# Kernel optimization log

Measured on AMD Instinct MI355X. Metric: run time of the kernel, lower is better.

## Reference

```python
import jax, jax.numpy as jnp
import numpy as np

LAMBDA = 1.0

def _patches3x3(x):
    # x: [B, C, H, W] -> [B, C, 3, 3, H, W] of 3x3 zero-padded neighborhoods
    B, C, H, W = x.shape
    xp = jnp.pad(x, ((0, 0), (0, 0), (1, 1), (1, 1)))
    rows = []
    for i in range(3):
        cols = [xp[:, :, i:i + H, j:j + W] for j in range(3)]
        rows.append(jnp.stack(cols, axis=2))  # [B, C, 3, H, W]
    return jnp.stack(rows, axis=2)  # [B, C, 3, 3, H, W]


def setup_inputs() -> dict:
    key = jax.random.key(0)
    kU, kV, kW = jax.random.split(key, 3)
    B, Cin, Cout, H, W = 8, 16, 16, 224, 224
    U = jax.random.normal(kU, (B, Cin, H, W), dtype=jnp.float32)
    V = jax.random.normal(kV, (B, Cin, H, W), dtype=jnp.float32)
    # nn.init.uniform_(weight, -0.1, 0.1)
    weight = jax.random.uniform(kW, (Cout, Cin, 3, 3), dtype=jnp.float32,
                                minval=-0.1, maxval=0.1)
    return {"U": U, "V": V, "weight": weight}


def reference(U, V, weight):
    # u1_u2 / v1_v2: 3x3 neighborhood minus center pixel, per input channel
    u_diff = _patches3x3(U) - U[:, :, None, None, :, :]  # [B,C,3,3,H,W]
    v_diff = _patches3x3(V) - V[:, :, None, None, :, :]
    inv_l2 = 1.0 / (LAMBDA * LAMBDA)
    # S = 1 / sqrt(1 + |v1-v2|^2 / lambda^2)
    S = jax.lax.rsqrt(1.0 + v_diff * v_diff * inv_l2)
    # out[b,o,h,w] = sum_{c,ki,kj} weight[o,c,ki,kj] * S * u_diff
    out = jnp.einsum('ocij,bcijhw->bohw', weight, S * u_diff)
    return out
```

## Files before the change

kernel.cpp:

```cpp
#include <hip/hip_runtime.h>


constexpr int Bn = 8, Ci = 16, Co = 16, H = 224, W = 224;
constexpr int HW = H * W;

typedef _Float16 f16x8 __attribute__((ext_vector_type(8)));
typedef float    f32x4 __attribute__((ext_vector_type(4)));

template <bool EDGE>
__device__ __forceinline__ void load_row(const float* __restrict__ plane,
                                         int h, int w, float r[3]) {
  if (!EDGE) {
    const float* q = plane + h * W + w;
    r[0] = q[-1]; r[1] = q[0]; r[2] = q[1];
  } else {
    if ((unsigned)h < (unsigned)H) {
      const float* q = plane + h * W + w;
      r[0] = (w >= 1)     ? q[-1] : 0.0f;
      r[1] = q[0];
      r[2] = (w + 1 < W) ? q[1] : 0.0f;
    } else {
      r[0] = 0.0f; r[1] = 0.0f; r[2] = 0.0f;
    }
  }
}

template <bool EDGE>
__device__ __forceinline__ void sdconv_wave(
    const float* __restrict__ U, const float* __restrict__ V,
    const float* __restrict__ Wg, float* __restrict__ Out,
    int b, int h0, int w0, int lane) {
  const int px = lane & 15;
  const int cg = lane >> 4;

  const int w = w0 + px;

  f16x8 bfrag[4];
#pragma unroll
  for (int kc = 0; kc < 4; ++kc) {
    const int c = 4 * kc + cg;
    const float* wp = Wg + (px * Ci + c) * 9;
#pragma unroll
    for (int j = 0; j < 8; ++j) {
      const int tap = (j < 4) ? j : j + 1;
      bfrag[kc][j] = (_Float16)wp[tap];
    }
  }

  f32x4 d[4];
#pragma unroll
  for (int r = 0; r < 4; ++r) { d[r][0] = 0.f; d[r][1] = 0.f; d[r][2] = 0.f; d[r][3] = 0.f; }

#pragma unroll
  for (int kc = 0; kc < 4; ++kc) {
    const int c = 4 * kc + cg;
    const float* up = U + ((size_t)(b * Ci + c)) * HW;
    const float* vp = V + ((size_t)(b * Ci + c)) * HW;

    float u[3][3], v[3][3];
    load_row<EDGE>(up, h0 - 1, w, u[0]);
    load_row<EDGE>(vp, h0 - 1, w, v[0]);
    load_row<EDGE>(up, h0,     w, u[1]);
    load_row<EDGE>(vp, h0,     w, v[1]);

#pragma unroll
    for (int r = 0; r < 4; ++r) {
      load_row<EDGE>(up, h0 + r + 1, w, u[2]);
      load_row<EDGE>(vp, h0 + r + 1, w, v[2]);

      const float uc = u[1][1], vc = v[1][1];
      f16x8 a;
      int j = 0;
#pragma unroll
      for (int dh = 0; dh < 3; ++dh) {
#pragma unroll
        for (int dw = 0; dw < 3; ++dw) {
          if (dh == 1 && dw == 1) continue;
          const float vd = v[dh][dw] - vc;
          const float s  = rsqrtf(fmaf(vd, vd, 1.0f));
          a[j++] = (_Float16)(s * (u[dh][dw] - uc));
        }
      }
      d[r] = __builtin_amdgcn_mfma_f32_16x16x32_f16(a, bfrag[kc], d[r], 0, 0, 0);

#pragma unroll
      for (int i = 0; i < 3; ++i) {
        u[0][i] = u[1][i]; u[1][i] = u[2][i];
        v[0][i] = v[1][i]; v[1][i] = v[2][i];
      }
    }
  }

  const int wst = w0 + 4 * cg;
  const int o   = px;
#pragma unroll
  for (int r = 0; r < 4; ++r) {
    float* op = Out + (((size_t)b * Co + o) * H + (h0 + r)) * W + wst;
    *reinterpret_cast<f32x4*>(op) = d[r];
  }
}

__global__ __launch_bounds__(128)
void sdconv_mfma(const float* __restrict__ U, const float* __restrict__ V,
                 const float* __restrict__ Wg, float* __restrict__ Out) {
  const int lane = threadIdx.x & 63;
  const int wv   = threadIdx.x >> 6;
  const int w0 = blockIdx.x * 16;
  const int h0 = blockIdx.y * 8 + wv * 4;
  const int b  = blockIdx.z;

  const bool edge = (blockIdx.x == 0) | (blockIdx.x == gridDim.x - 1) |
                    (blockIdx.y == 0) | (blockIdx.y == gridDim.y - 1);
  if (edge)
    sdconv_wave<true >(U, V, Wg, Out, b, h0, w0, lane);
  else
    sdconv_wave<false>(U, V, Wg, Out, b, h0, w0, lane);
}

extern "C" void kernel_launch(void* const* d_in, const int* in_sizes, int n_in,
                              void* d_out, int out_size, void* d_ws, size_t ws_size,
                              hipStream_t stream) {
  const float* U  = (const float*)d_in[0];
  const float* V  = (const float*)d_in[1];
  const float* Wg = (const float*)d_in[2];
  float* Out = (float*)d_out;

  dim3 grid(W / 16, H / 8, Bn);
  dim3 block(128);
  sdconv_mfma<<<grid, block, 0, stream>>>(U, V, Wg, Out);
}
```

Baseline: 125.7 us.

## Process eight rows per wave with channel-interleaved rolling window and raw rsq

Each wave now computes eight output rows instead of four, which halves the grid and reduces the redundant halo-row reloads per output row. The loop order is swapped so that each output row loads the new input row for all four channel groups first and then issues the four MFMAs. The rolling three-row window is indexed with modular slots instead of shifting registers. rsqrtf is replaced by the raw hardware rsq builtin to drop any extra precision handling. The trade-off is higher register pressure from holding eight accumulators and four channel windows, and fewer blocks available for occupancy.

After: 119.8 us. -4.7%, faster.

```diff
diff --git a/kernel.cpp b/kernel.cpp
--- a/kernel.cpp
+++ b/kernel.cpp
@@ -3,13 +3,14 @@
 
 constexpr int Bn = 8, Ci = 16, Co = 16, H = 224, W = 224;
 constexpr int HW = H * W;
+constexpr int ROWS = 8;
 
 typedef _Float16 f16x8 __attribute__((ext_vector_type(8)));
 typedef float    f32x4 __attribute__((ext_vector_type(4)));
 
 template <bool EDGE>
 __device__ __forceinline__ void load_row(const float* __restrict__ plane,
-                                         int h, int w, float r[3]) {
+                                         int h, int w, float* __restrict__ r) {
   if (!EDGE) {
     const float* q = plane + h * W + w;
     r[0] = q[-1]; r[1] = q[0]; r[2] = q[1];
@@ -32,8 +33,7 @@
     int b, int h0, int w0, int lane) {
   const int px = lane & 15;
   const int cg = lane >> 4;
-
-  const int w = w0 + px;
+  const int w  = w0 + px;
 
   f16x8 bfrag[4];
 #pragma unroll
@@ -47,28 +47,44 @@
     }
   }
 
-  f32x4 d[4];
+  f32x4 d[ROWS];
 #pragma unroll
-  for (int r = 0; r < 4; ++r) { d[r][0] = 0.f; d[r][1] = 0.f; d[r][2] = 0.f; d[r][3] = 0.f; }
+  for (int r = 0; r < ROWS; ++r) d[r] = (f32x4){0.f, 0.f, 0.f, 0.f};
 
+  const float* up[4];
+  const float* vp[4];
 #pragma unroll
   for (int kc = 0; kc < 4; ++kc) {
     const int c = 4 * kc + cg;
-    const float* up = U + ((size_t)(b * Ci + c)) * HW;
-    const float* vp = V + ((size_t)(b * Ci + c)) * HW;
+    up[kc] = U + ((size_t)(b * Ci + c)) * HW;
+    vp[kc] = V + ((size_t)(b * Ci + c)) * HW;
+  }
 
-    float u[3][3], v[3][3];
-    load_row<EDGE>(up, h0 - 1, w, u[0]);
-    load_row<EDGE>(vp, h0 - 1, w, v[0]);
-    load_row<EDGE>(up, h0,     w, u[1]);
-    load_row<EDGE>(vp, h0,     w, v[1]);
+  float u[4][3][3], v[4][3][3];
+#pragma unroll
+  for (int kc = 0; kc < 4; ++kc) {
+    load_row<EDGE>(up[kc], h0 - 1, w, u[kc][0]);
+    load_row<EDGE>(vp[kc], h0 - 1, w, v[kc][0]);
+    load_row<EDGE>(up[kc], h0,     w, u[kc][1]);
+    load_row<EDGE>(vp[kc], h0,     w, v[kc][1]);
+  }
 
 #pragma unroll
-    for (int r = 0; r < 4; ++r) {
-      load_row<EDGE>(up, h0 + r + 1, w, u[2]);
-      load_row<EDGE>(vp, h0 + r + 1, w, v[2]);
+  for (int r = 0; r < ROWS; ++r) {
+    const int st = r % 3;
+    const int sm = (r + 1) % 3;
+    const int sb = (r + 2) % 3;
 
-      const float uc = u[1][1], vc = v[1][1];
+#pragma unroll
+    for (int kc = 0; kc < 4; ++kc) {
+      load_row<EDGE>(up[kc], h0 + r + 1, w, u[kc][sb]);
+      load_row<EDGE>(vp[kc], h0 + r + 1, w, v[kc][sb]);
+    }
+
+#pragma unroll
+    for (int kc = 0; kc < 4; ++kc) {
+      const float uc = u[kc][sm][1], vc = v[kc][sm][1];
+      const int slot[3] = {st, sm, sb};
       f16x8 a;
       int j = 0;
 #pragma unroll
@@ -76,25 +92,19 @@
 #pragma unroll
         for (int dw = 0; dw < 3; ++dw) {
           if (dh == 1 && dw == 1) continue;
-          const float vd = v[dh][dw] - vc;
-          const float s  = rsqrtf(fmaf(vd, vd, 1.0f));
-          a[j++] = (_Float16)(s * (u[dh][dw] - uc));
+          const float vd = v[kc][slot[dh]][dw] - vc;
+          const float s  = __builtin_amdgcn_rsqf(fmaf(vd, vd, 1.0f));
+          a[j++] = (_Float16)(s * (u[kc][slot[dh]][dw] - uc));
         }
       }
       d[r] = __builtin_amdgcn_mfma_f32_16x16x32_f16(a, bfrag[kc], d[r], 0, 0, 0);
-
-#pragma unroll
-      for (int i = 0; i < 3; ++i) {
-        u[0][i] = u[1][i]; u[1][i] = u[2][i];
-        v[0][i] = v[1][i]; v[1][i] = v[2][i];
-      }
     }
   }
 
   const int wst = w0 + 4 * cg;
   const int o   = px;
 #pragma unroll
-  for (int r = 0; r < 4; ++r) {
+  for (int r = 0; r < ROWS; ++r) {
     float* op = Out + (((size_t)b * Co + o) * H + (h0 + r)) * W + wst;
     *reinterpret_cast<f32x4*>(op) = d[r];
   }
@@ -106,7 +116,7 @@
   const int lane = threadIdx.x & 63;
   const int wv   = threadIdx.x >> 6;
   const int w0 = blockIdx.x * 16;
-  const int h0 = blockIdx.y * 8 + wv * 4;
+  const int h0 = blockIdx.y * 16 + wv * ROWS;
   const int b  = blockIdx.z;
 
   const bool edge = (blockIdx.x == 0) | (blockIdx.x == gridDim.x - 1) |
@@ -125,7 +135,7 @@
   const float* Wg = (const float*)d_in[2];
   float* Out = (float*)d_out;
 
-  dim3 grid(W / 16, H / 8, Bn);
+  dim3 grid(W / 16, H / 16, Bn);
   dim3 block(128);
   sdconv_mfma<<<grid, block, 0, stream>>>(U, V, Wg, Out);
 }
```
